# Optimization experiments

Measured on AMD Instinct MI355X. Metric: run time of the kernel, lower is better.

Reference implementation:

```python
import jax, jax.numpy as jnp
import numpy as np

B, N, IN_F, OUT_F, H = 64, 256, 128, 128, 4
NEG_SLOPE = 0.2  # nn.LeakyReLU(dropout) -> slope 0.2


def setup_inputs() -> dict:
    key = jax.random.key(0)
    ks = jax.random.split(key, 10)
    h = jax.random.normal(ks[0], (B, N, IN_F), dtype=jnp.float32)
    projection_matrix = jax.random.normal(ks[1], (B, N, N), dtype=jnp.float32)
    similarity_matrix = jax.random.uniform(ks[2], (B, N, N), dtype=jnp.float32) * 2.0 - 1.0
    quadrant_matrix = jax.random.randint(ks[3], (B, N, N, 2), 0, 4, dtype=jnp.int32)
    # parameters (xavier-ish scaling)
    W = jax.random.normal(ks[4], (IN_F, OUT_F * H), dtype=jnp.float32) / np.sqrt(IN_F)
    a = jax.random.normal(ks[5], (H, 2 * OUT_F, 1), dtype=jnp.float32) / np.sqrt(2 * OUT_F)
    w_proj = jax.random.normal(ks[6], (OUT_F,), dtype=jnp.float32) / np.sqrt(OUT_F)
    w_sim = jax.random.normal(ks[7], (OUT_F,), dtype=jnp.float32) / np.sqrt(OUT_F)
    quadrant_bias = jax.random.normal(ks[8], (4, 4), dtype=jnp.float32) * 0.02
    W_concat = jax.random.normal(ks[9], (OUT_F * H, OUT_F), dtype=jnp.float32) / np.sqrt(OUT_F * H)
    return {"h": h, "projection_matrix": projection_matrix,
            "similarity_matrix": similarity_matrix, "quadrant_matrix": quadrant_matrix,
            "W": W, "a": a, "w_proj": w_proj, "w_sim": w_sim,
            "quadrant_bias": quadrant_bias, "W_concat": W_concat}


def reference(h, projection_matrix, similarity_matrix, quadrant_matrix,
              W, a, w_proj, w_sim, quadrant_bias, W_concat):
    b, n, _ = h.shape
    # Wh_heads: (B, H, N, F)
    Wh = (h @ W).reshape(b, n, H, OUT_F).transpose(0, 2, 1, 3)
    # GAT score: a^T [Wh_i || Wh_j] decomposes into two rank-1 terms
    a1, a2 = a[:, :OUT_F, 0], a[:, OUT_F:, 0]            # (H, F) each
    e_i = jnp.einsum('bhnf,hf->bhn', Wh, a1)
    e_j = jnp.einsum('bhnf,hf->bhn', Wh, a2)
    e = e_i[:, :, :, None] + e_j[:, :, None, :]          # (B, H, N, N)
    e = jnp.where(e > 0, e, NEG_SLOPE * e)               # leaky relu
    # projection bias: <Wh_i, proj[b,i,j] * w_proj> = (Wh_i . w_proj) * proj[b,i,j]
    s_proj = jnp.einsum('bhnf,f->bhn', Wh, w_proj)
    e = e + s_proj[:, :, :, None] * projection_matrix[:, None, :, :]
    # similarity bias, same factored form
    s_sim = jnp.einsum('bhnf,f->bhn', Wh, w_sim)
    e = e + s_sim[:, :, :, None] * similarity_matrix[:, None, :, :]
    # quadrant bias gather
    qb = quadrant_bias[quadrant_matrix[..., 0], quadrant_matrix[..., 1]]  # (B, N, N)
    e = e + qb[:, None, :, :]
    attn = jax.nn.softmax(e, axis=-1)                    # dropout is identity in eval
    h_prime = jnp.einsum('bhij,bhjf->bhif', attn, Wh)    # (B, H, N, F)
    h_prime = h_prime.transpose(0, 2, 1, 3).reshape(b, n, H * OUT_F) @ W_concat
    return jax.nn.elu(h_prime)
```

## Files before the change

### kernel.cpp

```cpp
#include <hip/hip_runtime.h>
#include <math.h>

#define BB 64
#define NN 256
#define IN_F 128
#define OF 128
#define HH 4
#define NEG_SLOPE 0.2f

typedef __attribute__((ext_vector_type(8))) short short8;
typedef __attribute__((ext_vector_type(4))) float f32x4;

#define MFMA16(a, b, c) __builtin_amdgcn_mfma_f32_16x16x32_bf16(a, b, c, 0, 0, 0)

__device__ inline unsigned short f2bf(float x) {
    unsigned u = __float_as_uint(x);
    u += 0x7fff + ((u >> 16) & 1);
    return (unsigned short)(u >> 16);
}

__global__ __launch_bounds__(256) void k0_convert(const float* __restrict__ h,
        const float* __restrict__ W, const float* __restrict__ Wc,
        unsigned short* __restrict__ h_bf, unsigned short* __restrict__ Wt,
        unsigned short* __restrict__ Wct) {
    __shared__ float hl[16][516];
    int blk = blockIdx.x, t = threadIdx.x;
    if (blk < 2048) {
        int idx = blk * 256 + t;
        float4 v = ((const float4*)h)[idx];
        ushort4 o;
        o.x = f2bf(v.x); o.y = f2bf(v.y); o.z = f2bf(v.z); o.w = f2bf(v.w);
        ((ushort4*)h_bf)[idx] = o;
    } else if (blk < 2056) {
        int k0 = (blk - 2048) * 16;
#pragma unroll
        for (int it = 0; it < 8; it++) {
            int li = it * 256 + t;
            int row = li >> 7, col4 = li & 127;
            float4 v = ((const float4*)(W + (size_t)(k0 + row) * 512))[col4];
            *(float4*)&hl[row][col4 * 4] = v;
        }
        __syncthreads();
#pragma unroll
        for (int cc = 0; cc < 2; cc++) {
            int c = t * 2 + cc;
            short8 s0, s1;
#pragma unroll
            for (int k = 0; k < 8; k++) s0[k] = (short)f2bf(hl[k][c]);
#pragma unroll
            for (int k = 0; k < 8; k++) s1[k] = (short)f2bf(hl[k + 8][c]);
            unsigned short* dst = Wt + (size_t)c * 128 + k0;
            *(short8*)dst = s0;
            *(short8*)(dst + 8) = s1;
        }
    } else {
        int k0 = (blk - 2056) * 16;
#pragma unroll
        for (int it = 0; it < 2; it++) {
            int li = it * 256 + t;
            int row = li >> 5, col4 = li & 31;
            float4 v = ((const float4*)(Wc + (size_t)(k0 + row) * 128))[col4];
            *(float4*)&hl[row][col4 * 4] = v;
        }
        __syncthreads();
        if (t < 128) {
            int c = t;
            short8 s0, s1;
#pragma unroll
            for (int k = 0; k < 8; k++) s0[k] = (short)f2bf(hl[k][c]);
#pragma unroll
            for (int k = 0; k < 8; k++) s1[k] = (short)f2bf(hl[k + 8][c]);
            unsigned short* dst = Wct + (size_t)c * 512 + k0;
            *(short8*)dst = s0;
            *(short8*)(dst + 8) = s1;
        }
    }
}

__global__ __launch_bounds__(256) void k1_wh(const unsigned short* __restrict__ h_bf,
        const unsigned short* __restrict__ Wt, const float* __restrict__ a,
        const float* __restrict__ w_proj, const float* __restrict__ w_sim,
        unsigned short* __restrict__ Wht, float* __restrict__ ei,
        float* __restrict__ ej, float* __restrict__ sp, float* __restrict__ ss) {
    __shared__ float a1s[512], a2s[512], wps[128], wss[128];
    int l = blockIdx.x;
    int xcd = l & 7, m = l >> 3;
    int b = xcd + ((m >> 2) << 3);
    int n0 = (m & 3) * 64;
    int t = threadIdx.x;
    for (int idx = t; idx < 512; idx += 256) {
        int hh = idx >> 7, f = idx & 127;
        a1s[idx] = a[hh * 256 + f];
        a2s[idx] = a[hh * 256 + 128 + f];
    }
    if (t < 128) { wps[t] = w_proj[t]; wss[t] = w_sim[t]; }
    __syncthreads();

    int w = t >> 6, lane = t & 63;
    int cc = lane & 15, g = lane >> 4;

    short8 bh[4][4];
#pragma unroll
    for (int tn = 0; tn < 4; tn++)
#pragma unroll
        for (int ks = 0; ks < 4; ks++)
            bh[tn][ks] = *(const short8*)(h_bf +
                ((size_t)(b * NN + n0 + tn * 16 + cc)) * IN_F + ks * 32 + g * 8);

    float q0[4] = {0.f,0.f,0.f,0.f}, q1[4] = {0.f,0.f,0.f,0.f};
    float q2[4] = {0.f,0.f,0.f,0.f}, q3[4] = {0.f,0.f,0.f,0.f};
    unsigned short* whb = Wht + (size_t)(b * HH + w) * OF * NN;

#pragma unroll
    for (int tf = 0; tf < 8; tf++) {
        short8 aw[4];
#pragma unroll
        for (int ks = 0; ks < 4; ks++)
            aw[ks] = *(const short8*)(Wt +
                (size_t)(w * 128 + tf * 16 + cc) * IN_F + ks * 32 + g * 8);
        f32x4 acc[4];
#pragma unroll
        for (int tn = 0; tn < 4; tn++) acc[tn] = (f32x4)(0.f);
#pragma unroll
        for (int tn = 0; tn < 4; tn++)
#pragma unroll
            for (int ks = 0; ks < 4; ks++)
                acc[tn] = MFMA16(aw[ks], bh[tn][ks], acc[tn]);

        float a1v[4], a2v[4], wpv[4], wsv[4];
#pragma unroll
        for (int r = 0; r < 4; r++) {
            int f = tf * 16 + g * 4 + r;
            a1v[r] = a1s[w * 128 + f];
            a2v[r] = a2s[w * 128 + f];
            wpv[r] = wps[f];
            wsv[r] = wss[f];
        }
#pragma unroll
        for (int tn = 0; tn < 4; tn++)
#pragma unroll
            for (int r = 0; r < 4; r++) {
                float v = acc[tn][r];
                q0[tn] += v * a1v[r];
                q1[tn] += v * a2v[r];
                q2[tn] += v * wpv[r];
                q3[tn] += v * wsv[r];
                whb[(size_t)(tf * 16 + g * 4 + r) * NN + n0 + tn * 16 + cc] = f2bf(v);
            }
    }

#pragma unroll
    for (int tn = 0; tn < 4; tn++) {
        float p0 = q0[tn], p1 = q1[tn], p2 = q2[tn], p3 = q3[tn];
        p0 += __shfl_xor(p0, 16); p0 += __shfl_xor(p0, 32);
        p1 += __shfl_xor(p1, 16); p1 += __shfl_xor(p1, 32);
        p2 += __shfl_xor(p2, 16); p2 += __shfl_xor(p2, 32);
        p3 += __shfl_xor(p3, 16); p3 += __shfl_xor(p3, 32);
        if (g == 0) {
            size_t idx = (size_t)(b * HH + w) * NN + n0 + tn * 16 + cc;
            ei[idx] = p0; ej[idx] = p1; sp[idx] = p2; ss[idx] = p3;
        }
    }
}

__global__ __launch_bounds__(256) void k2_fused(
        const float* __restrict__ proj, const float* __restrict__ sim,
        const int* __restrict__ qm, const float* __restrict__ qbias,
        const float* __restrict__ ei, const float* __restrict__ ej,
        const float* __restrict__ sp, const float* __restrict__ ss,
        const unsigned short* __restrict__ Wht, const unsigned short* __restrict__ Wct,
        float* __restrict__ out) {
    __shared__ __align__(16) char at_lds[32768];
    __shared__ __align__(16) char hp_lds[16384];
    __shared__ float eis[HH][16], sps[HH][16], sss[HH][16];
    __shared__ float qb_s[16];
    float* ejs = (float*)hp_lds;

    int l = blockIdx.x;
    int xcd = l & 7, m = l >> 3;
    int b = xcd + ((m >> 4) << 3);
    int i0 = (m & 15) * 16;
    int t = threadIdx.x;
    int wave = t >> 6, lane = t & 63;

    for (int c = t; c < HH * NN; c += 256)
        ejs[c] = ej[(size_t)b * HH * NN + c];
    if (t < 64) {
        int hh = t >> 4, ii = t & 15;
        size_t base = ((size_t)b * HH + hh) * NN + i0 + ii;
        eis[hh][ii] = ei[base]; sps[hh][ii] = sp[base]; sss[hh][ii] = ss[base];
    }
    if (t < 16) qb_s[t] = qbias[t];
    __syncthreads();

    int j0 = lane * 4;
    float4 P4[4], S4[4];
    int4 qa[4], qc[4];
#pragma unroll
    for (int rr = 0; rr < 4; rr++) {
        int i = i0 + wave * 4 + rr;
        size_t rb = ((size_t)b * NN + i) * NN + j0;
        P4[rr] = *(const float4*)&proj[rb];
        S4[rr] = *(const float4*)&sim[rb];
        qa[rr] = *(const int4*)&qm[rb * 2];
        qc[rr] = *(const int4*)&qm[rb * 2 + 4];
    }
#pragma unroll
    for (int rr = 0; rr < 4; rr++) {
        int ii = wave * 4 + rr;
        float qb0 = qb_s[qa[rr].x * 4 + qa[rr].y], qb1 = qb_s[qa[rr].z * 4 + qa[rr].w];
        float qb2 = qb_s[qc[rr].x * 4 + qc[rr].y], qb3 = qb_s[qc[rr].z * 4 + qc[rr].w];
        float e[HH][4];
#pragma unroll
        for (int hh = 0; hh < HH; hh++) {
            float4 ej4 = *(const float4*)&ejs[hh * 256 + j0];
            float bi = eis[hh][ii], spv = sps[hh][ii], ssv = sss[hh][ii];
            float x;
            x = bi + ej4.x; x = x > 0.f ? x : NEG_SLOPE * x; e[hh][0] = x + spv * P4[rr].x + ssv * S4[rr].x + qb0;
            x = bi + ej4.y; x = x > 0.f ? x : NEG_SLOPE * x; e[hh][1] = x + spv * P4[rr].y + ssv * S4[rr].y + qb1;
            x = bi + ej4.z; x = x > 0.f ? x : NEG_SLOPE * x; e[hh][2] = x + spv * P4[rr].z + ssv * S4[rr].z + qb2;
            x = bi + ej4.w; x = x > 0.f ? x : NEG_SLOPE * x; e[hh][3] = x + spv * P4[rr].w + ssv * S4[rr].w + qb3;
        }
        float mx[HH];
#pragma unroll
        for (int hh = 0; hh < HH; hh++)
            mx[hh] = fmaxf(fmaxf(e[hh][0], e[hh][1]), fmaxf(e[hh][2], e[hh][3]));
#pragma unroll
        for (int off = 32; off; off >>= 1)
#pragma unroll
            for (int hh = 0; hh < HH; hh++)
                mx[hh] = fmaxf(mx[hh], __shfl_xor(mx[hh], off));
        float s[HH];
#pragma unroll
        for (int hh = 0; hh < HH; hh++) {
            e[hh][0] = __expf(e[hh][0] - mx[hh]);
            e[hh][1] = __expf(e[hh][1] - mx[hh]);
            e[hh][2] = __expf(e[hh][2] - mx[hh]);
            e[hh][3] = __expf(e[hh][3] - mx[hh]);
            s[hh] = (e[hh][0] + e[hh][1]) + (e[hh][2] + e[hh][3]);
        }
#pragma unroll
        for (int off = 32; off; off >>= 1)
#pragma unroll
            for (int hh = 0; hh < HH; hh++) s[hh] += __shfl_xor(s[hh], off);
#pragma unroll
        for (int hh = 0; hh < HH; hh++) {
            float inv = 1.0f / s[hh];
            ushort4 pk;
            pk.x = f2bf(e[hh][0] * inv);
            pk.y = f2bf(e[hh][1] * inv);
            pk.z = f2bf(e[hh][2] * inv);
            pk.w = f2bf(e[hh][3] * inv);
            int off2 = hh * 8192 + ii * 512 + ((j0 * 2) ^ ((ii & 7) << 4));
            *(ushort4*)(at_lds + off2) = pk;
        }
    }
    __syncthreads();

    int w = wave;
    int row = lane & 15, g = lane >> 4;
    short8 af[8];
#pragma unroll
    for (int ks = 0; ks < 8; ks++) {
        int off = w * 8192 + row * 512 + ((((ks * 32 + g * 8) * 2)) ^ ((row & 7) << 4));
        af[ks] = *(const short8*)(at_lds + off);
    }
    f32x4 acc[8];
#pragma unroll
    for (int ft = 0; ft < 8; ft++) acc[ft] = (f32x4)(0.f);
    const unsigned short* whb = Wht + (size_t)(b * HH + w) * OF * NN;
#pragma unroll
    for (int ft = 0; ft < 8; ft++) {
        const unsigned short* wb = whb + (size_t)(ft * 16 + row) * NN + g * 8;
#pragma unroll
        for (int ks = 0; ks < 8; ks++) {
            short8 bf = *(const short8*)(wb + ks * 32);
            acc[ft] = MFMA16(af[ks], bf, acc[ft]);
        }
    }
#pragma unroll
    for (int ft = 0; ft < 8; ft++)
#pragma unroll
        for (int r = 0; r < 4; r++) {
            int i = g * 4 + r;
            int kf = w * 128 + ft * 16 + row;
            int off = i * 1024 + ((kf * 2) ^ ((i & 7) << 4));
            *(unsigned short*)(hp_lds + off) = f2bf(acc[ft][r]);
        }
    __syncthreads();

    short8 ah[16];
#pragma unroll
    for (int ks = 0; ks < 16; ks++) {
        int off = row * 1024 + (((ks * 32 + g * 8) * 2) ^ ((row & 7) << 4));
        ah[ks] = *(const short8*)(hp_lds + off);
    }
    f32x4 o2[2];
    o2[0] = (f32x4)(0.f); o2[1] = (f32x4)(0.f);
#pragma unroll
    for (int ct = 0; ct < 2; ct++) {
        int c = (w * 2 + ct) * 16 + row;
        const unsigned short* wc = Wct + (size_t)c * 512 + g * 8;
#pragma unroll
        for (int ks = 0; ks < 16; ks++) {
            short8 bf = *(const short8*)(wc + ks * 32);
            o2[ct] = MFMA16(ah[ks], bf, o2[ct]);
        }
    }
#pragma unroll
    for (int ct = 0; ct < 2; ct++)
#pragma unroll
        for (int r = 0; r < 4; r++) {
            float v = o2[ct][r];
            v = v > 0.f ? v : expm1f(v);
            int i = i0 + g * 4 + r;
            int c = (w * 2 + ct) * 16 + row;
            out[((size_t)b * NN + i) * OF + c] = v;
        }
}

extern "C" void kernel_launch(void* const* d_in, const int* in_sizes, int n_in,
                              void* d_out, int out_size, void* d_ws, size_t ws_size,
                              hipStream_t stream) {
    const float* h      = (const float*)d_in[0];
    const float* proj   = (const float*)d_in[1];
    const float* sim    = (const float*)d_in[2];
    const int*   qm     = (const int*)d_in[3];
    const float* W      = (const float*)d_in[4];
    const float* a      = (const float*)d_in[5];
    const float* w_proj = (const float*)d_in[6];
    const float* w_sim  = (const float*)d_in[7];
    const float* qbias  = (const float*)d_in[8];
    const float* Wc     = (const float*)d_in[9];
    float* out = (float*)d_out;

    unsigned short* h_bf = (unsigned short*)d_ws;
    unsigned short* Wt   = h_bf + (size_t)BB * NN * IN_F;
    unsigned short* Wct  = Wt + 512 * 128;
    unsigned short* Wht  = Wct + 128 * 512;
    float* ei = (float*)(Wht + (size_t)BB * HH * OF * NN);
    float* ej = ei + (size_t)BB * HH * NN;
    float* sp = ej + (size_t)BB * HH * NN;
    float* ss = sp + (size_t)BB * HH * NN;

    k0_convert<<<2088, 256, 0, stream>>>(h, W, Wc, h_bf, Wt, Wct);
    k1_wh<<<BB * 4, 256, 0, stream>>>(h_bf, Wt, a, w_proj, w_sim, Wht, ei, ej, sp, ss);
    k2_fused<<<BB * 16, 256, 0, stream>>>(proj, sim, qm, qbias, ei, ej, sp, ss, Wht, Wct, out);
}
```

Baseline: 185.0 us.

## Pack quadrant indices to bytes and fuse h conversion into Wh kernel

The prep kernel now packs the int32 quadrant pairs into one byte index per element instead of converting h to bf16. k1 converts h to bf16 directly into swizzled LDS, and it uses more blocks with a transposed MFMA so Wh can be stored as vectorized ushort4. k2 reads the 1-byte quadrant indices instead of 8 bytes per element and reuses the attention LDS buffer for h_prime. The idea is to cut global traffic in k2 and drop the h_bf round trip. The cost is that k0 still has to read the full int32 quadrant matrix, and k2 gains an extra barrier.

```diff
diff --git a/kernel.cpp b/kernel.cpp
--- a/kernel.cpp
+++ b/kernel.cpp
@@ -19,18 +19,22 @@
     return (unsigned short)(u >> 16);
 }
 
-__global__ __launch_bounds__(256) void k0_convert(const float* __restrict__ h,
+__global__ __launch_bounds__(256) void k0_prep(const int* __restrict__ qm,
         const float* __restrict__ W, const float* __restrict__ Wc,
-        unsigned short* __restrict__ h_bf, unsigned short* __restrict__ Wt,
+        unsigned char* __restrict__ qidx, unsigned short* __restrict__ Wt,
         unsigned short* __restrict__ Wct) {
     __shared__ float hl[16][516];
     int blk = blockIdx.x, t = threadIdx.x;
     if (blk < 2048) {
-        int idx = blk * 256 + t;
-        float4 v = ((const float4*)h)[idx];
-        ushort4 o;
-        o.x = f2bf(v.x); o.y = f2bf(v.y); o.z = f2bf(v.z); o.w = f2bf(v.w);
-        ((ushort4*)h_bf)[idx] = o;
+        const int4* qp = (const int4*)qm;
+        size_t base = (size_t)blk * 1024;
+#pragma unroll
+        for (int it = 0; it < 4; it++) {
+            size_t i4 = base + it * 256 + t;
+            int4 v = qp[i4];
+            unsigned short pk = (unsigned short)((v.x * 4 + v.y) | ((v.z * 4 + v.w) << 8));
+            ((unsigned short*)qidx)[i4] = pk;
+        }
     } else if (blk < 2056) {
         int k0 = (blk - 2048) * 16;
 #pragma unroll
@@ -77,16 +81,15 @@
     }
 }
 
-__global__ __launch_bounds__(256) void k1_wh(const unsigned short* __restrict__ h_bf,
+__global__ __launch_bounds__(256) void k1_wh(const float* __restrict__ h,
         const unsigned short* __restrict__ Wt, const float* __restrict__ a,
         const float* __restrict__ w_proj, const float* __restrict__ w_sim,
         unsigned short* __restrict__ Wht, float* __restrict__ ei,
         float* __restrict__ ej, float* __restrict__ sp, float* __restrict__ ss) {
+    __shared__ __align__(16) unsigned char hs[8192];
     __shared__ float a1s[512], a2s[512], wps[128], wss[128];
     int l = blockIdx.x;
-    int xcd = l & 7, m = l >> 3;
-    int b = xcd + ((m >> 2) << 3);
-    int n0 = (m & 3) * 64;
+    int b = l >> 3, n0 = (l & 7) * 32;
     int t = threadIdx.x;
     for (int idx = t; idx < 512; idx += 256) {
         int hh = idx >> 7, f = idx & 127;
@@ -94,87 +97,99 @@
         a2s[idx] = a[hh * 256 + 128 + f];
     }
     if (t < 128) { wps[t] = w_proj[t]; wss[t] = w_sim[t]; }
+    {
+        const float4* hsrc = (const float4*)(h + ((size_t)b * NN + n0) * IN_F);
+#pragma unroll
+        for (int it = 0; it < 4; it++) {
+            int li = it * 256 + t;
+            float4 v = hsrc[li];
+            int row = li >> 5, col4 = li & 31;
+            ushort4 o;
+            o.x = f2bf(v.x); o.y = f2bf(v.y); o.z = f2bf(v.z); o.w = f2bf(v.w);
+            *(ushort4*)(hs + row * 256 + ((col4 * 8) ^ ((row & 7) << 4))) = o;
+        }
+    }
     __syncthreads();
 
     int w = t >> 6, lane = t & 63;
     int cc = lane & 15, g = lane >> 4;
 
-    short8 bh[4][4];
-#pragma unroll
-    for (int tn = 0; tn < 4; tn++)
+    short8 bh[2][4];
+#pragma unroll
+    for (int tn = 0; tn < 2; tn++) {
+        int row = tn * 16 + cc;
 #pragma unroll
         for (int ks = 0; ks < 4; ks++)
-            bh[tn][ks] = *(const short8*)(h_bf +
-                ((size_t)(b * NN + n0 + tn * 16 + cc)) * IN_F + ks * 32 + g * 8);
-
-    float q0[4] = {0.f,0.f,0.f,0.f}, q1[4] = {0.f,0.f,0.f,0.f};
-    float q2[4] = {0.f,0.f,0.f,0.f}, q3[4] = {0.f,0.f,0.f,0.f};
+            bh[tn][ks] = *(const short8*)(hs + row * 256 + ((ks * 64 + g * 16) ^ ((row & 7) << 4)));
+    }
+
+    float q[2][4][4] = {{{0.f}}};
     unsigned short* whb = Wht + (size_t)(b * HH + w) * OF * NN;
 
 #pragma unroll
     for (int tf = 0; tf < 8; tf++) {
+        int f = tf * 16 + cc;
         short8 aw[4];
 #pragma unroll
         for (int ks = 0; ks < 4; ks++)
-            aw[ks] = *(const short8*)(Wt +
-                (size_t)(w * 128 + tf * 16 + cc) * IN_F + ks * 32 + g * 8);
-        f32x4 acc[4];
-#pragma unroll
-        for (int tn = 0; tn < 4; tn++) acc[tn] = (f32x4)(0.f);
-#pragma unroll
-        for (int tn = 0; tn < 4; tn++)
-#pragma unroll
-            for (int ks = 0; ks < 4; ks++)
-                acc[tn] = MFMA16(aw[ks], bh[tn][ks], acc[tn]);
-
-        float a1v[4], a2v[4], wpv[4], wsv[4];
-#pragma unroll
-        for (int r = 0; r < 4; r++) {
-            int f = tf * 16 + g * 4 + r;
-            a1v[r] = a1s[w * 128 + f];
-            a2v[r] = a2s[w * 128 + f];
-            wpv[r] = wps[f];
-            wsv[r] = wss[f];
-        }
-#pragma unroll
-        for (int tn = 0; tn < 4; tn++)
+            aw[ks] = *(const short8*)(Wt + (size_t)(w * 128 + f) * IN_F + ks * 32 + g * 8);
+        f32x4 acc[2];
+        acc[0] = (f32x4)(0.f); acc[1] = (f32x4)(0.f);
+#pragma unroll
+        for (int ks = 0; ks < 4; ks++) {
+            acc[0] = MFMA16(bh[0][ks], aw[ks], acc[0]);
+            acc[1] = MFMA16(bh[1][ks], aw[ks], acc[1]);
+        }
+        float c1 = a1s[w * 128 + f], c2 = a2s[w * 128 + f];
+        float c3 = wps[f], c4 = wss[f];
+#pragma unroll
+        for (int tn = 0; tn < 2; tn++) {
+            ushort4 o;
+            o.x = f2bf(acc[tn][0]); o.y = f2bf(acc[tn][1]);
+            o.z = f2bf(acc[tn][2]); o.w = f2bf(acc[tn][3]);
+            *(ushort4*)(whb + (size_t)f * NN + n0 + tn * 16 + g * 4) = o;
 #pragma unroll
             for (int r = 0; r < 4; r++) {
                 float v = acc[tn][r];
-                q0[tn] += v * a1v[r];
-                q1[tn] += v * a2v[r];
-                q2[tn] += v * wpv[r];
-                q3[tn] += v * wsv[r];
-                whb[(size_t)(tf * 16 + g * 4 + r) * NN + n0 + tn * 16 + cc] = f2bf(v);
+                q[tn][0][r] += v * c1; q[tn][1][r] += v * c2;
+                q[tn][2][r] += v * c3; q[tn][3][r] += v * c4;
             }
-    }
-
-#pragma unroll
-    for (int tn = 0; tn < 4; tn++) {
-        float p0 = q0[tn], p1 = q1[tn], p2 = q2[tn], p3 = q3[tn];
-        p0 += __shfl_xor(p0, 16); p0 += __shfl_xor(p0, 32);
-        p1 += __shfl_xor(p1, 16); p1 += __shfl_xor(p1, 32);
-        p2 += __shfl_xor(p2, 16); p2 += __shfl_xor(p2, 32);
-        p3 += __shfl_xor(p3, 16); p3 += __shfl_xor(p3, 32);
-        if (g == 0) {
-            size_t idx = (size_t)(b * HH + w) * NN + n0 + tn * 16 + cc;
-            ei[idx] = p0; ej[idx] = p1; sp[idx] = p2; ss[idx] = p3;
+        }
+    }
+#pragma unroll
+    for (int tn = 0; tn < 2; tn++)
+#pragma unroll
+        for (int ty = 0; ty < 4; ty++)
+#pragma unroll
+            for (int r = 0; r < 4; r++) {
+                float v = q[tn][ty][r];
+                v += __shfl_xor(v, 1); v += __shfl_xor(v, 2);
+                v += __shfl_xor(v, 4); v += __shfl_xor(v, 8);
+                q[tn][ty][r] = v;
+            }
+    if (cc == 0) {
+#pragma unroll
+        for (int tn = 0; tn < 2; tn++) {
+            size_t base = (size_t)(b * HH + w) * NN + n0 + tn * 16 + g * 4;
+            *(float4*)&ei[base] = make_float4(q[tn][0][0], q[tn][0][1], q[tn][0][2], q[tn][0][3]);
+            *(float4*)&ej[base] = make_float4(q[tn][1][0], q[tn][1][1], q[tn][1][2], q[tn][1][3]);
+            *(float4*)&sp[base] = make_float4(q[tn][2][0], q[tn][2][1], q[tn][2][2], q[tn][2][3]);
+            *(float4*)&ss[base] = make_float4(q[tn][3][0], q[tn][3][1], q[tn][3][2], q[tn][3][3]);
         }
     }
 }
 
 __global__ __launch_bounds__(256) void k2_fused(
         const float* __restrict__ proj, const float* __restrict__ sim,
-        const int* __restrict__ qm, const float* __restrict__ qbias,
+        const unsigned char* __restrict__ qidx, const float* __restrict__ qbias,
         const float* __restrict__ ei, const float* __restrict__ ej,
         const float* __restrict__ sp, const float* __restrict__ ss,
         const unsigned short* __restrict__ Wht, const unsigned short* __restrict__ Wct,
         float* __restrict__ out) {
     __shared__ __align__(16) char at_lds[32768];
-    __shared__ __align__(16) char hp_lds[16384];
+    __shared__ __align__(16) float ejs[1024];
     __shared__ float eis[HH][16], sps[HH][16], sss[HH][16];
     __shared__ float qb_s[16];
-    float* ejs = (float*)hp_lds;
 
     int l = blockIdx.x;
     int xcd = l & 7, m = l >> 3;
@@ -195,21 +210,22 @@
 
     int j0 = lane * 4;
     float4 P4[4], S4[4];
-    int4 qa[4], qc[4];
+    unsigned qi[4];
 #pragma unroll
     for (int rr = 0; rr < 4; rr++) {
         int i = i0 + wave * 4 + rr;
         size_t rb = ((size_t)b * NN + i) * NN + j0;
         P4[rr] = *(const float4*)&proj[rb];
         S4[rr] = *(const float4*)&sim[rb];
-        qa[rr] = *(const int4*)&qm[rb * 2];
-        qc[rr] = *(const int4*)&qm[rb * 2 + 4];
+        qi[rr] = *(const unsigned*)(qidx + rb);
     }
 #pragma unroll
     for (int rr = 0; rr < 4; rr++) {
         int ii = wave * 4 + rr;
-        float qb0 = qb_s[qa[rr].x * 4 + qa[rr].y], qb1 = qb_s[qa[rr].z * 4 + qa[rr].w];
-        float qb2 = qb_s[qc[rr].x * 4 + qc[rr].y], qb3 = qb_s[qc[rr].z * 4 + qc[rr].w];
+        float qb0 = qb_s[qi[rr] & 15];
+        float qb1 = qb_s[(qi[rr] >> 8) & 15];
+        float qb2 = qb_s[(qi[rr] >> 16) & 15];
+        float qb3 = qb_s[(qi[rr] >> 24) & 15];
         float e[HH][4];
 #pragma unroll
         for (int hh = 0; hh < HH; hh++) {
@@ -262,9 +278,11 @@
     short8 af[8];
 #pragma unroll
     for (int ks = 0; ks < 8; ks++) {
-        int off = w * 8192 + row * 512 + ((((ks * 32 + g * 8) * 2)) ^ ((row & 7) << 4));
+        int off = w * 8192 + row * 512 + ((ks * 64 + g * 16) ^ ((row & 7) << 4));
         af[ks] = *(const short8*)(at_lds + off);
     }
+    __syncthreads();
+
     f32x4 acc[8];
 #pragma unroll
     for (int ft = 0; ft < 8; ft++) acc[ft] = (f32x4)(0.f);
@@ -285,15 +303,15 @@
             int i = g * 4 + r;
             int kf = w * 128 + ft * 16 + row;
             int off = i * 1024 + ((kf * 2) ^ ((i & 7) << 4));
-            *(unsigned short*)(hp_lds + off) = f2bf(acc[ft][r]);
+            *(unsigned short*)(at_lds + off) = f2bf(acc[ft][r]);
         }
     __syncthreads();
 
     short8 ah[16];
 #pragma unroll
     for (int ks = 0; ks < 16; ks++) {
-        int off = row * 1024 + (((ks * 32 + g * 8) * 2) ^ ((row & 7) << 4));
-        ah[ks] = *(const short8*)(hp_lds + off);
+        int off = row * 1024 + ((ks * 64 + g * 16) ^ ((row & 7) << 4));
+        ah[ks] = *(const short8*)(at_lds + off);
     }
     f32x4 o2[2];
     o2[0] = (f32x4)(0.f); o2[1] = (f32x4)(0.f);
@@ -334,16 +352,16 @@
     const float* Wc     = (const float*)d_in[9];
     float* out = (float*)d_out;
 
-    unsigned short* h_bf = (unsigned short*)d_ws;
-    unsigned short* Wt   = h_bf + (size_t)BB * NN * IN_F;
-    unsigned short* Wct  = Wt + 512 * 128;
-    unsigned short* Wht  = Wct + 128 * 512;
+    unsigned short* Wt  = (unsigned short*)d_ws;
+    unsigned short* Wct = Wt + 512 * 128;
+    unsigned short* Wht = Wct + 128 * 512;
     float* ei = (float*)(Wht + (size_t)BB * HH * OF * NN);
     float* ej = ei + (size_t)BB * HH * NN;
     float* sp = ej + (size_t)BB * HH * NN;
     float* ss = sp + (size_t)BB * HH * NN;
-
-    k0_convert<<<2088, 256, 0, stream>>>(h, W, Wc, h_bf, Wt, Wct);
-    k1_wh<<<BB * 4, 256, 0, stream>>>(h_bf, Wt, a, w_proj, w_sim, Wht, ei, ej, sp, ss);
-    k2_fused<<<BB * 16, 256, 0, stream>>>(proj, sim, qm, qbias, ei, ej, sp, ss, Wht, Wct, out);
-}
+    unsigned char* qidx = (unsigned char*)(ss + (size_t)BB * HH * NN);
+
+    k0_prep<<<2088, 256, 0, stream>>>(qm, W, Wc, qidx, Wt, Wct);
+    k1_wh<<<512, 256, 0, stream>>>(h, Wt, a, w_proj, w_sim, Wht, ei, ej, sp, ss);
+    k2_fused<<<BB * 16, 256, 0, stream>>>(proj, sim, qidx, qbias, ei, ej, sp, ss, Wht, Wct, out);
+}
```

After: 198.5 us. 7.3% more time.
